# Performance work log

Hardware: AMD Instinct MI355X
Metric: run time of the kernel (lower is better)

The kernel has to match this reference:

```python
import jax, jax.numpy as jnp
import numpy as np
import math

B, T, DIM, NH, NKV, HD = 1, 2048, 1024, 16, 8, 64
N_REP = NH // NKV
LAMBDA_INIT = 0.8 - 0.6 * math.exp(-0.3)  # layer_idx = 0
EPS = 1e-5


def _rope(t, cos, sin):
    # t: (B, T, H, HD); cos/sin: (T, HD//2)
    tr = t.reshape(t.shape[:-1] + (HD // 2, 2))
    r, i = tr[..., 0], tr[..., 1]
    c = cos[None, :, None, :]
    s = sin[None, :, None, :]
    out_r = r * c - i * s
    out_i = r * s + i * c
    return jnp.stack([out_r, out_i], axis=-1).reshape(t.shape)


def setup_inputs():
    key = jax.random.key(0)
    ks = jax.random.split(key, 9)
    x = jax.random.normal(ks[0], (B, T, DIM), jnp.float32)
    inv_freq = 1.0 / (10000.0 ** (np.arange(0, HD, 2, dtype=np.float32) / HD))
    angles = np.outer(np.arange(T, dtype=np.float32), inv_freq)  # (T, HD//2)
    freqs_cos = jnp.asarray(np.cos(angles), jnp.float32)
    freqs_sin = jnp.asarray(np.sin(angles), jnp.float32)
    wq = jax.random.normal(ks[1], (2 * NH * HD, DIM), jnp.float32) * 0.02
    wk = jax.random.normal(ks[2], (2 * NKV * HD, DIM), jnp.float32) * 0.02
    wv = jax.random.normal(ks[3], (NKV * HD, DIM), jnp.float32) * 0.02
    wo = jax.random.normal(ks[4], (DIM, NH * HD), jnp.float32) * 0.02
    lambda_q1 = jax.random.normal(ks[5], (HD,), jnp.float32) * 0.1
    lambda_k1 = jax.random.normal(ks[6], (HD,), jnp.float32) * 0.1
    lambda_q2 = jax.random.normal(ks[7], (HD,), jnp.float32) * 0.1
    lambda_k2 = jax.random.normal(ks[8], (HD,), jnp.float32) * 0.1
    return dict(x=x, freqs_cos=freqs_cos, freqs_sin=freqs_sin, wq=wq, wk=wk,
                wv=wv, wo=wo, lambda_q1=lambda_q1, lambda_k1=lambda_k1,
                lambda_q2=lambda_q2, lambda_k2=lambda_k2)


def reference(x, freqs_cos, freqs_sin, wq, wk, wv, wo,
              lambda_q1, lambda_k1, lambda_q2, lambda_k2):
    Bc, Tc, C = x.shape
    q = (x @ wq.T).reshape(Bc, Tc, NH, 2, HD)
    k = (x @ wk.T).reshape(Bc, Tc, NKV, 2, HD)
    v = (x @ wv.T).reshape(Bc, Tc, NKV, HD)
    q1, q2 = q[..., 0, :], q[..., 1, :]
    k1, k2 = k[..., 0, :], k[..., 1, :]
    q1 = _rope(q1, freqs_cos, freqs_sin)
    k1 = _rope(k1, freqs_cos, freqs_sin)
    q2 = _rope(q2, freqs_cos, freqs_sin)
    k2 = _rope(k2, freqs_cos, freqs_sin)
    # GQA: repeat each kv head n_rep times consecutively
    k1 = jnp.repeat(k1, N_REP, axis=2)
    k2 = jnp.repeat(k2, N_REP, axis=2)
    v = jnp.repeat(v, N_REP, axis=2)
    # (B, H, T, HD)
    q1, q2 = jnp.swapaxes(q1, 1, 2), jnp.swapaxes(q2, 1, 2)
    k1, k2 = jnp.swapaxes(k1, 1, 2), jnp.swapaxes(k2, 1, 2)
    v = jnp.swapaxes(v, 1, 2)
    scale = 1.0 / math.sqrt(HD)
    mask = jnp.tril(jnp.ones((Tc, Tc), bool))

    def attn_probs(qh, kh):
        s = jnp.einsum('bhtd,bhsd->bhts', qh, kh) * scale
        s = jnp.where(mask[None, None], s, -jnp.inf)
        return jax.nn.softmax(s, axis=-1)

    a1 = attn_probs(q1, k1)
    a2 = attn_probs(q2, k2)
    lam = (jnp.exp(jnp.sum(lambda_q1 * lambda_k1))
           - jnp.exp(jnp.sum(lambda_q2 * lambda_k2)) + LAMBDA_INIT)
    y = jnp.einsum('bhts,bhsd->bhtd', a1 - lam * a2, v)  # (B,H,T,HD)
    y = jnp.swapaxes(y, 1, 2)  # (B,T,H,HD)
    # GroupNorm(num_groups=NH, affine=False) on (B,C,T): normalize per (batch, head)
    # over (T, HD) elements.
    mean = y.mean(axis=(1, 3), keepdims=True)
    var = y.var(axis=(1, 3), keepdims=True)
    y = (y - mean) / jnp.sqrt(var + EPS)
    y = y.reshape(Bc, Tc, C) * (1.0 - LAMBDA_INIT)
    return y @ wo.T
```

## Files before the change

### kernel.cpp

```cpp
#include <hip/hip_runtime.h>
#include <hip/hip_bf16.h>
#include <cstdint>

#define T_SEQ 2048
#define DIM   1024
#define NHEAD 16
#define NKVH  8
#define HDIM  64
#define QKVN  3584

static constexpr float LAMBDA_INIT_F = 0.3555090675909693f;
static constexpr float ONE_MINUS_LI  = 0.6444909324090307f;
static constexpr float QSCALE_EXP2   = 0.1803368801111144f;

typedef __bf16 bf16x8 __attribute__((ext_vector_type(8)));
typedef float  f32x4  __attribute__((ext_vector_type(4)));

static __device__ __forceinline__ ushort f2bf(float f) {
  union { float f; uint32_t u; } x; x.f = f;
  uint32_t u = x.u;
  uint32_t r = (u + 0x7fffu + ((u >> 16) & 1u)) >> 16;
  return (ushort)r;
}
static __device__ __forceinline__ float bf2f(ushort u) {
  union { uint32_t u; float f; } x; x.u = ((uint32_t)u) << 16; return x.f;
}
static __device__ __forceinline__ f32x4 zero4() {
  f32x4 z = {0.f, 0.f, 0.f, 0.f}; return z;
}
static __device__ __forceinline__ bf16x8 ldfrag128(const ushort* p) {
  union { bf16x8 v; uint4 u; } r;
  r.u = *(const uint4*)p;
  return r.v;
}
static __device__ __forceinline__ void gll16(const ushort* g, ushort* l) {
  __builtin_amdgcn_global_load_lds(
      (const __attribute__((address_space(1))) uint32_t*)g,
      (__attribute__((address_space(3))) uint32_t*)l, 16, 0, 0);
}

__global__ void cvt_all(const float* __restrict__ x,  const float* __restrict__ wq,
                        const float* __restrict__ wk, const float* __restrict__ wv,
                        const float* __restrict__ wo,
                        ushort* __restrict__ xb, ushort* __restrict__ Wb,
                        ushort* __restrict__ Wob) {
  int g = (blockIdx.x * 256 + threadIdx.x) * 4;
  float4 v; ushort* dst; int j;
  if (g < 2097152) {
    v = *(const float4*)(x + g); dst = xb; j = g;
  } else if (g < 5767168) {
    j = g - 2097152;
    const float* src = (j < 2097152) ? (wq + j)
                     : (j < 3145728) ? (wk + (j - 2097152))
                                     : (wv + (j - 3145728));
    v = *(const float4*)src; dst = Wb;
  } else {
    j = g - 5767168;
    v = *(const float4*)(wo + j); dst = Wob;
  }
  int q = (j & 31) >> 2;
  int jp = (j & ~31) + ((q & 3) << 3) + ((q >> 2) << 2);
  ushort4 o4;
  o4.x = f2bf(v.x); o4.y = f2bf(v.y); o4.z = f2bf(v.z); o4.w = f2bf(v.w);
  *(ushort4*)(dst + jp) = o4;
}

__global__ void lam_kernel(const float* __restrict__ lq1, const float* __restrict__ lk1,
                           const float* __restrict__ lq2, const float* __restrict__ lk2,
                           float* __restrict__ lam) {
  int lane = threadIdx.x;
  float p1 = lq1[lane] * lk1[lane];
  float p2 = lq2[lane] * lk2[lane];
  #pragma unroll
  for (int off = 32; off >= 1; off >>= 1) {
    p1 += __shfl_down(p1, off);
    p2 += __shfl_down(p2, off);
  }
  if (lane == 0) *lam = expf(p1) - expf(p2) + LAMBDA_INIT_F;
}

template<int BF16OUT>
__global__ __launch_bounds__(256) void gemm_bt(const ushort* __restrict__ A,
                                               const ushort* __restrict__ W,
                                               void* __restrict__ Cout,
                                               int M, int N, int K) {
  __shared__ __align__(16) ushort As[2 * 128 * 32];
  __shared__ __align__(16) ushort Ws[2 * 128 * 32];
  const int tid  = threadIdx.x;
  const int lane = tid & 63;
  const int w    = tid >> 6;
  const int wr   = w >> 1, wc = w & 1;
  const int nwg = gridDim.x * gridDim.y;
  int id  = blockIdx.x * gridDim.y + blockIdx.y;
  int sw  = (id & 7) * (nwg >> 3) + (id >> 3);
  const int bm = (sw % gridDim.y) * 128;
  const int bn = (sw / gridDim.y) * 128;
  const int fr = lane & 15;
  const int fg = (lane >> 4) * 4;
  const int g8 = (lane >> 4) * 8;

  f32x4 acc[4][4];
  #pragma unroll
  for (int m = 0; m < 4; ++m)
    #pragma unroll
    for (int n = 0; n < 4; ++n) acc[m][n] = zero4();

  const int col  = (lane & 3) * 8;
  const int row0 = w * 16 + (lane >> 2);
  const int row1 = row0 + 64;
  const ushort* ga0 = A + (size_t)(bm + row0) * K + col;
  const ushort* ga1 = A + (size_t)(bm + row1) * K + col;
  const ushort* gw0 = W + (size_t)(bn + row0) * K + col;
  const ushort* gw1 = W + (size_t)(bn + row1) * K + col;
  ushort* la0 = As + (w * 512);
  ushort* la1 = As + (w * 512) + 2048;
  ushort* la2 = As + 4096 + (w * 512);
  ushort* la3 = As + 4096 + (w * 512) + 2048;
  ushort* lw0 = Ws + (w * 512);
  ushort* lw1 = Ws + (w * 512) + 2048;
  ushort* lw2 = Ws + 4096 + (w * 512);
  ushort* lw3 = Ws + 4096 + (w * 512) + 2048;

  for (int k0 = 0; k0 < K; k0 += 64) {
    gll16(ga0 + k0,      la0);
    gll16(ga1 + k0,      la1);
    gll16(ga0 + k0 + 32, la2);
    gll16(ga1 + k0 + 32, la3);
    gll16(gw0 + k0,      lw0);
    gll16(gw1 + k0,      lw1);
    gll16(gw0 + k0 + 32, lw2);
    gll16(gw1 + k0 + 32, lw3);
    __syncthreads();
    #pragma unroll
    for (int kk = 0; kk < 2; ++kk) {
      bf16x8 af[4], bfr[4];
      #pragma unroll
      for (int m = 0; m < 4; ++m)
        af[m]  = ldfrag128(&As[kk*4096 + (wr*64 + m*16 + fr) * 32 + g8]);
      #pragma unroll
      for (int n = 0; n < 4; ++n)
        bfr[n] = ldfrag128(&Ws[kk*4096 + (wc*64 + n*16 + fr) * 32 + g8]);
      #pragma unroll
      for (int m = 0; m < 4; ++m)
        #pragma unroll
        for (int n = 0; n < 4; ++n)
          acc[m][n] = __builtin_amdgcn_mfma_f32_16x16x32_bf16(af[m], bfr[n], acc[m][n], 0, 0, 0);
    }
    __syncthreads();
  }

  #pragma unroll
  for (int m = 0; m < 4; ++m)
    #pragma unroll
    for (int n = 0; n < 4; ++n)
      #pragma unroll
      for (int i = 0; i < 4; ++i) {
        int row = bm + wr*64 + m*16 + fg + i;
        int colg = bn + wc*64 + n*16 + fr;
        float v = acc[m][n][i];
        if (BF16OUT) ((ushort*)Cout)[(size_t)row * N + colg] = f2bf(v);
        else         ((float*)Cout)[(size_t)row * N + colg]  = v;
      }
}

__global__ void reorg(const ushort* __restrict__ QKV, ushort* __restrict__ Qr,
                      ushort* __restrict__ Kr, ushort* __restrict__ Vt,
                      const float* __restrict__ fc, const float* __restrict__ fs) {
  int idx = blockIdx.x * 256 + threadIdx.x;
  if (idx < 786432) {
    int nheads, col_off; ushort* dst; float scale; int id;
    if (idx < 524288) { id = idx * 4; nheads = NHEAD; col_off = 0; dst = Qr; scale = QSCALE_EXP2; }
    else { id = (idx - 524288) * 4; nheads = NKVH; col_off = 2048; dst = Kr; scale = 1.0f; }
    int per_t = nheads * 64;
    int t  = id / per_t;
    int r  = id - t * per_t;
    int hh = r >> 6;
    int c2 = (r >> 5) & 1;
    int j  = r & 31;
    int cl = col_off + hh * 128 + c2 * 64 + 2 * j;
    uint4 raw = *(const uint4*)(QKV + (size_t)t * QKVN + cl);
    const ushort* rp = (const ushort*)&raw;
    float c4[4], s4[4];
    *(float4*)c4 = *(const float4*)(fc + t * 32 + j);
    *(float4*)s4 = *(const float4*)(fs + t * 32 + j);
    ushort outv[8];
    #pragma unroll
    for (int p = 0; p < 4; ++p) {
      float rv = bf2f(rp[2*p]), iv = bf2f(rp[2*p + 1]);
      outv[2*p]     = f2bf((rv * c4[p] - iv * s4[p]) * scale);
      outv[2*p + 1] = f2bf((rv * s4[p] + iv * c4[p]) * scale);
    }
    int d0 = 2 * j;
    int o  = d0 & 31;
    int q0 = o >> 2;
    int s0 = ((q0 & 3) << 3) + ((q0 >> 2) << 2);
    int s1 = (((q0+1) & 3) << 3) + (((q0+1) >> 2) << 2);
    size_t ob = ((size_t)(c2 * nheads + hh) * T_SEQ + t) * HDIM + (d0 & ~31);
    *(uint2*)(dst + ob + s0) = *(const uint2*)(outv);
    *(uint2*)(dst + ob + s1) = *(const uint2*)(outv + 4);
  } else {
    int id = (idx - 786432) * 8;
    int t = id & (T_SEQ - 1);
    int rest = id >> 11;
    ushort outv[8];
    #pragma unroll
    for (int p = 0; p < 8; ++p) outv[p] = QKV[(size_t)(t + p) * QKVN + 3072 + rest];
    int o  = t & 31;
    int q0 = o >> 2;
    int s0 = ((q0 & 3) << 3) + ((q0 >> 2) << 2);
    int s1 = (((q0+1) & 3) << 3) + (((q0+1) >> 2) << 2);
    size_t ob = (size_t)rest * T_SEQ + (t & ~31);
    *(uint2*)(Vt + ob + s0) = *(const uint2*)(outv);
    *(uint2*)(Vt + ob + s1) = *(const uint2*)(outv + 4);
  }
}

__global__ __launch_bounds__(256, 2) void attn_kernel(const ushort* __restrict__ Qr,
                                                      const ushort* __restrict__ Kr,
                                                      const ushort* __restrict__ Vt,
                                                      const float* __restrict__ lamp,
                                                      float* __restrict__ Yf,
                                                      float* __restrict__ part) {
  const int bx = blockIdx.x;
  const int h  = bx & 15;
  const int jb = bx >> 4;
  const int qb = (jb < 16) ? (31 - jb) : (jb - 16);
  const int kh = h >> 1;
  const int tid = threadIdx.x;
  const int lane = tid & 63;
  const int w   = tid >> 6;
  const int st  = w >> 1;
  const int qh  = w & 1;
  const int fr  = lane & 15;
  const int fg  = (lane >> 4) * 4;
  const int g8  = (lane >> 4) * 8;

  __shared__ float ob[64 * 64];
  __shared__ float sb[8];

  bf16x8 qf[2][2];
  #pragma unroll
  for (int qs = 0; qs < 2; ++qs) {
    const int row = qb * 64 + qh * 32 + qs * 16 + fr;
    const ushort* qp = Qr + ((size_t)(st * NHEAD + h) * T_SEQ + row) * HDIM;
    qf[qs][0] = ldfrag128(qp + g8);
    qf[qs][1] = ldfrag128(qp + 32 + g8);
  }

  float m_[2] = {-__builtin_inff(), -__builtin_inff()};
  float l_[2] = {0.f, 0.f};
  f32x4 o_[2][4];
  #pragma unroll
  for (int qs = 0; qs < 2; ++qs)
    #pragma unroll
    for (int dn = 0; dn < 4; ++dn) o_[qs][dn] = zero4();

  const ushort* Kbase = Kr + ((size_t)(st * NKVH + kh) * T_SEQ + fr) * HDIM + g8;
  const ushort* Vbase = Vt + ((size_t)(kh * 64 + fr) * T_SEQ) + g8;

#define SINGLE_TILE(KT, DOMASK) do {                                          \
    const int kvb_ = (KT) * 64;                                               \
    bf16x8 kf_[4][2], vf_[4][2];                                              \
    _Pragma("unroll")                                                         \
    for (int n_ = 0; n_ < 4; ++n_) {                                          \
      const ushort* kp_ = Kbase + (size_t)(kvb_ + n_ * 16) * HDIM;            \
      kf_[n_][0] = ldfrag128(kp_);                                            \
      kf_[n_][1] = ldfrag128(kp_ + 32);                                       \
      const ushort* vp_ = Vbase + (size_t)(n_ * 16) * T_SEQ + kvb_;           \
      vf_[n_][0] = ldfrag128(vp_);                                            \
      vf_[n_][1] = ldfrag128(vp_ + 32);                                       \
    }                                                                         \
    float sv_[2][4][4];                                                       \
    __builtin_amdgcn_s_setprio(1);                                            \
    _Pragma("unroll")                                                         \
    for (int n_ = 0; n_ < 4; ++n_) {                                          \
      f32x4 a0_ = zero4(), a1_ = zero4();                                     \
      _Pragma("unroll")                                                       \
      for (int ks_ = 0; ks_ < 2; ++ks_) {                                     \
        a0_ = __builtin_amdgcn_mfma_f32_16x16x32_bf16(kf_[n_][ks_], qf[0][ks_], a0_, 0, 0, 0); \
        a1_ = __builtin_amdgcn_mfma_f32_16x16x32_bf16(kf_[n_][ks_], qf[1][ks_], a1_, 0, 0, 0); \
      }                                                                       \
      _Pragma("unroll")                                                       \
      for (int i_ = 0; i_ < 4; ++i_) { sv_[0][n_][i_] = a0_[i_]; sv_[1][n_][i_] = a1_[i_]; } \
    }                                                                         \
    __builtin_amdgcn_s_setprio(0);                                            \
    if (DOMASK) {                                                             \
      _Pragma("unroll")                                                       \
      for (int qs_ = 0; qs_ < 2; ++qs_) {                                     \
        const int qloc_ = qh*32 + qs_*16 + fr;                                \
        _Pragma("unroll")                                                     \
        for (int n_ = 0; n_ < 4; ++n_)                                        \
          _Pragma("unroll")                                                   \
          for (int i_ = 0; i_ < 4; ++i_)                                      \
            if (n_*16 + fg + i_ > qloc_) sv_[qs_][n_][i_] = -__builtin_inff();\
      }                                                                       \
    }                                                                         \
    bf16x8 pa_[2][2];                                                         \
    _Pragma("unroll")                                                         \
    for (int qs_ = 0; qs_ < 2; ++qs_) {                                       \
      float rm_ = -__builtin_inff();                                          \
      _Pragma("unroll")                                                       \
      for (int n_ = 0; n_ < 4; ++n_)                                          \
        _Pragma("unroll")                                                     \
        for (int i_ = 0; i_ < 4; ++i_) rm_ = fmaxf(rm_, sv_[qs_][n_][i_]);    \
      rm_ = fmaxf(rm_, __shfl_xor(rm_, 16));                                  \
      rm_ = fmaxf(rm_, __shfl_xor(rm_, 32));                                  \
      if (!__all(rm_ <= m_[qs_] + 8.f)) {                                     \
        float mnew_ = fmaxf(m_[qs_], rm_);                                    \
        float sc_ = __builtin_amdgcn_exp2f(m_[qs_] - mnew_);                  \
        m_[qs_] = mnew_;                                                      \
        l_[qs_] *= sc_;                                                       \
        float scs_[4];                                                        \
        _Pragma("unroll")                                                     \
        for (int i_ = 0; i_ < 4; ++i_) scs_[i_] = __shfl(sc_, fg + i_);       \
        _Pragma("unroll")                                                     \
        for (int dn_ = 0; dn_ < 4; ++dn_)                                     \
          _Pragma("unroll")                                                   \
          for (int i_ = 0; i_ < 4; ++i_) o_[qs_][dn_][i_] *= scs_[i_];        \
      }                                                                       \
      float rs_ = 0.f;                                                        \
      _Pragma("unroll")                                                       \
      for (int n_ = 0; n_ < 4; ++n_)                                          \
        _Pragma("unroll")                                                     \
        for (int i_ = 0; i_ < 4; ++i_) {                                      \
          float p_ = __builtin_amdgcn_exp2f(sv_[qs_][n_][i_] - m_[qs_]);      \
          sv_[qs_][n_][i_] = p_; rs_ += p_;                                   \
        }                                                                     \
      rs_ += __shfl_xor(rs_, 16);                                             \
      rs_ += __shfl_xor(rs_, 32);                                             \
      l_[qs_] += rs_;                                                         \
      _Pragma("unroll")                                                       \
      for (int ks_ = 0; ks_ < 2; ++ks_)                                       \
        _Pragma("unroll")                                                     \
        for (int n2_ = 0; n2_ < 2; ++n2_)                                     \
          _Pragma("unroll")                                                   \
          for (int i_ = 0; i_ < 4; ++i_)                                      \
            pa_[qs_][ks_][n2_*4 + i_] = (__bf16)sv_[qs_][2*ks_ + n2_][i_];    \
    }                                                                         \
    __builtin_amdgcn_s_setprio(1);                                            \
    _Pragma("unroll")                                                         \
    for (int ks_ = 0; ks_ < 2; ++ks_)                                         \
      _Pragma("unroll")                                                       \
      for (int dn_ = 0; dn_ < 4; ++dn_) {                                     \
        o_[0][dn_] = __builtin_amdgcn_mfma_f32_16x16x32_bf16(pa_[0][ks_], vf_[dn_][ks_], o_[0][dn_], 0, 0, 0); \
        o_[1][dn_] = __builtin_amdgcn_mfma_f32_16x16x32_bf16(pa_[1][ks_], vf_[dn_][ks_], o_[1][dn_], 0, 0, 0); \
      }                                                                       \
    __builtin_amdgcn_s_setprio(0);                                            \
  } while (0)

  const int nnd = qb;
  int kt = 0;
  for (; kt + 1 < nnd; kt += 2) {
    const int ka = kt * 64, kb = ka + 64;
    bf16x8 kfA[4][2], vfA[4][2], kfB[4][2], vfB[4][2];
    #pragma unroll
    for (int n = 0; n < 4; ++n) {
      const ushort* kpA = Kbase + (size_t)(ka + n * 16) * HDIM;
      const ushort* kpB = Kbase + (size_t)(kb + n * 16) * HDIM;
      kfA[n][0] = ldfrag128(kpA);  kfA[n][1] = ldfrag128(kpA + 32);
      kfB[n][0] = ldfrag128(kpB);  kfB[n][1] = ldfrag128(kpB + 32);
      const ushort* vpA = Vbase + (size_t)(n * 16) * T_SEQ + ka;
      vfA[n][0] = ldfrag128(vpA);  vfA[n][1] = ldfrag128(vpA + 32);
      const ushort* vpB = vpA + 64;
      vfB[n][0] = ldfrag128(vpB);  vfB[n][1] = ldfrag128(vpB + 32);
    }
    float svA[2][4][4], svB[2][4][4];
    __builtin_amdgcn_s_setprio(1);
    #pragma unroll
    for (int n = 0; n < 4; ++n) {
      f32x4 a0 = zero4(), a1 = zero4(), b0 = zero4(), b1 = zero4();
      #pragma unroll
      for (int ks = 0; ks < 2; ++ks) {
        a0 = __builtin_amdgcn_mfma_f32_16x16x32_bf16(kfA[n][ks], qf[0][ks], a0, 0, 0, 0);
        a1 = __builtin_amdgcn_mfma_f32_16x16x32_bf16(kfA[n][ks], qf[1][ks], a1, 0, 0, 0);
        b0 = __builtin_amdgcn_mfma_f32_16x16x32_bf16(kfB[n][ks], qf[0][ks], b0, 0, 0, 0);
        b1 = __builtin_amdgcn_mfma_f32_16x16x32_bf16(kfB[n][ks], qf[1][ks], b1, 0, 0, 0);
      }
      #pragma unroll
      for (int i = 0; i < 4; ++i) {
        svA[0][n][i] = a0[i]; svA[1][n][i] = a1[i];
        svB[0][n][i] = b0[i]; svB[1][n][i] = b1[i];
      }
    }
    __builtin_amdgcn_s_setprio(0);

    bf16x8 paA[2][2], paB[2][2];
    #pragma unroll
    for (int qs = 0; qs < 2; ++qs) {
      float rm = -__builtin_inff();
      #pragma unroll
      for (int n = 0; n < 4; ++n)
        #pragma unroll
        for (int i = 0; i < 4; ++i) {
          rm = fmaxf(rm, svA[qs][n][i]);
          rm = fmaxf(rm, svB[qs][n][i]);
        }
      rm = fmaxf(rm, __shfl_xor(rm, 16));
      rm = fmaxf(rm, __shfl_xor(rm, 32));
      if (!__all(rm <= m_[qs] + 8.f)) {
        float mnew = fmaxf(m_[qs], rm);
        float sc = __builtin_amdgcn_exp2f(m_[qs] - mnew);
        m_[qs] = mnew;
        l_[qs] *= sc;
        float scs[4];
        #pragma unroll
        for (int i = 0; i < 4; ++i) scs[i] = __shfl(sc, fg + i);
        #pragma unroll
        for (int dn = 0; dn < 4; ++dn)
          #pragma unroll
          for (int i = 0; i < 4; ++i) o_[qs][dn][i] *= scs[i];
      }
      float rs = 0.f;
      #pragma unroll
      for (int n = 0; n < 4; ++n)
        #pragma unroll
        for (int i = 0; i < 4; ++i) {
          float pA = __builtin_amdgcn_exp2f(svA[qs][n][i] - m_[qs]);
          float pB = __builtin_amdgcn_exp2f(svB[qs][n][i] - m_[qs]);
          svA[qs][n][i] = pA; svB[qs][n][i] = pB;
          rs += pA + pB;
        }
      rs += __shfl_xor(rs, 16);
      rs += __shfl_xor(rs, 32);
      l_[qs] += rs;
      #pragma unroll
      for (int ks = 0; ks < 2; ++ks)
        #pragma unroll
        for (int n2 = 0; n2 < 2; ++n2)
          #pragma unroll
          for (int i = 0; i < 4; ++i) {
            paA[qs][ks][n2*4 + i] = (__bf16)svA[qs][2*ks + n2][i];
            paB[qs][ks][n2*4 + i] = (__bf16)svB[qs][2*ks + n2][i];
          }
    }

    __builtin_amdgcn_s_setprio(1);
    #pragma unroll
    for (int ks = 0; ks < 2; ++ks)
      #pragma unroll
      for (int dn = 0; dn < 4; ++dn) {
        o_[0][dn] = __builtin_amdgcn_mfma_f32_16x16x32_bf16(paA[0][ks], vfA[dn][ks], o_[0][dn], 0, 0, 0);
        o_[1][dn] = __builtin_amdgcn_mfma_f32_16x16x32_bf16(paA[1][ks], vfA[dn][ks], o_[1][dn], 0, 0, 0);
      }
    #pragma unroll
    for (int ks = 0; ks < 2; ++ks)
      #pragma unroll
      for (int dn = 0; dn < 4; ++dn) {
        o_[0][dn] = __builtin_amdgcn_mfma_f32_16x16x32_bf16(paB[0][ks], vfB[dn][ks], o_[0][dn], 0, 0, 0);
        o_[1][dn] = __builtin_amdgcn_mfma_f32_16x16x32_bf16(paB[1][ks], vfB[dn][ks], o_[1][dn], 0, 0, 0);
      }
    __builtin_amdgcn_s_setprio(0);
  }
  if (kt < nnd) { SINGLE_TILE(kt, 0); ++kt; }
  SINGLE_TILE(qb, 1);
#undef SINGLE_TILE

  float iq[2][4];
  #pragma unroll
  for (int qs = 0; qs < 2; ++qs) {
    float inv = __builtin_amdgcn_rcpf(l_[qs]);
    #pragma unroll
    for (int i = 0; i < 4; ++i) iq[qs][i] = __shfl(inv, fg + i);
  }
  __syncthreads();
  if (st == 1) {
    #pragma unroll
    for (int qs = 0; qs < 2; ++qs)
      #pragma unroll
      for (int dn = 0; dn < 4; ++dn)
        #pragma unroll
        for (int i = 0; i < 4; ++i)
          ob[(qh*32 + qs*16 + fg + i)*64 + dn*16 + fr] = o_[qs][dn][i] * iq[qs][i];
  }
  __syncthreads();
  if (st == 0) {
    const float lam = *lamp;
    float s = 0.f, s2 = 0.f;
    #pragma unroll
    for (int qs = 0; qs < 2; ++qs)
      #pragma unroll
      for (int dn = 0; dn < 4; ++dn)
        #pragma unroll
        for (int i = 0; i < 4; ++i) {
          int r64 = qh*32 + qs*16 + fg + i;
          int d   = dn*16 + fr;
          float v = o_[qs][dn][i] * iq[qs][i] - lam * ob[r64*64 + d];
          Yf[(size_t)(qb*64 + r64) * DIM + h*64 + d] = v;
          s += v; s2 += v * v;
        }
    #pragma unroll
    for (int off = 1; off <= 32; off <<= 1) {
      s  += __shfl_xor(s, off);
      s2 += __shfl_xor(s2, off);
    }
    if (lane == 0) { sb[w] = s; sb[4 + w] = s2; }
  }
  __syncthreads();
  if (tid == 0) {
    part[bx]       = sb[0] + sb[1];
    part[512 + bx] = sb[4] + sb[5];
  }
}

__global__ void stats_final(const float* __restrict__ part, float* __restrict__ stat) {
  int hh = threadIdx.x;
  if (hh < 16) {
    float S = 0.f, S2 = 0.f;
    #pragma unroll
    for (int j = 0; j < 32; ++j) { S += part[j*16 + hh]; S2 += part[512 + j*16 + hh]; }
    const float N = (float)(T_SEQ * HDIM);
    float mean = S / N;
    float var  = S2 / N - mean * mean;
    stat[hh]      = mean;
    stat[16 + hh] = rsqrtf(var + 1e-5f);
  }
}

__global__ void norm_cvt(const float* __restrict__ Y, const float* __restrict__ stats,
                         ushort* __restrict__ Yb) {
  int idx = (blockIdx.x * 256 + threadIdx.x) * 4;
  int col = idx & (DIM - 1);
  int h = col >> 6;
  float mean = stats[h], isd = stats[16 + h] * ONE_MINUS_LI;
  float4 v = *(const float4*)(Y + idx);
  ushort4 o4;
  o4.x = f2bf((v.x - mean) * isd);
  o4.y = f2bf((v.y - mean) * isd);
  o4.z = f2bf((v.z - mean) * isd);
  o4.w = f2bf((v.w - mean) * isd);
  int q = (col & 31) >> 2;
  int idxp = (idx & ~31) + ((q & 3) << 3) + ((q >> 2) << 2);
  *(ushort4*)(Yb + idxp) = o4;
}

extern "C" void kernel_launch(void* const* d_in, const int* in_sizes, int n_in,
                              void* d_out, int out_size, void* d_ws, size_t ws_size,
                              hipStream_t stream) {
  const float* x   = (const float*)d_in[0];
  const float* fc  = (const float*)d_in[1];
  const float* fs  = (const float*)d_in[2];
  const float* wq  = (const float*)d_in[3];
  const float* wk  = (const float*)d_in[4];
  const float* wv  = (const float*)d_in[5];
  const float* wo  = (const float*)d_in[6];
  const float* lq1 = (const float*)d_in[7];
  const float* lk1 = (const float*)d_in[8];
  const float* lq2 = (const float*)d_in[9];
  const float* lk2 = (const float*)d_in[10];
  float* out = (float*)d_out;

  char* ws = (char*)d_ws;
  const size_t OFF_WOB  = 0;
  const size_t OFF_XB   = 2097152;
  const size_t OFF_WB   = 6291456;
  const size_t OFF_QKV  = 13631488;
  const size_t OFF_QR   = 28311552;
  const size_t OFF_KR   = 36700160;
  const size_t OFF_VT   = 40894464;
  const size_t OFF_Y    = 18874368;
  const size_t OFF_YB   = 42991616;
  const size_t OFF_ST   = 47185920;

  ushort* xb   = (ushort*)(ws + OFF_XB);
  ushort* Wb   = (ushort*)(ws + OFF_WB);
  ushort* Wob  = (ushort*)(ws + OFF_WOB);
  ushort* QKVb = (ushort*)(ws + OFF_QKV);
  ushort* Qr   = (ushort*)(ws + OFF_QR);
  ushort* Kr   = (ushort*)(ws + OFF_KR);
  ushort* Vt   = (ushort*)(ws + OFF_VT);
  float*  Yf   = (float*)(ws + OFF_Y);
  ushort* Yb   = (ushort*)(ws + OFF_YB);
  float*  stat = (float*)(ws + OFF_ST);
  float*  lamp = stat + 32;
  float*  part = stat + 64;

  cvt_all<<<6656, 256, 0, stream>>>(x, wq, wk, wv, wo, xb, Wb, Wob);
  lam_kernel<<<1, 64, 0, stream>>>(lq1, lk1, lq2, lk2, lamp);

  gemm_bt<1><<<dim3(QKVN/128, T_SEQ/128), 256, 0, stream>>>(xb, Wb, QKVb, T_SEQ, QKVN, DIM);

  reorg<<<3584, 256, 0, stream>>>(QKVb, Qr, Kr, Vt, fc, fs);

  attn_kernel<<<512, 256, 0, stream>>>(Qr, Kr, Vt, lamp, Yf, part);

  stats_final<<<1, 64, 0, stream>>>(part, stat);
  norm_cvt<<<2048, 256, 0, stream>>>(Yf, stat, Yb);

  gemm_bt<0><<<dim3(DIM/128, T_SEQ/128), 256, 0, stream>>>(Yb, Wob, out, T_SEQ, DIM, DIM);
}
```

Measured before the change: 141.2 us.

## Store Q/K/V in MFMA fragment-tiled layout for contiguous per-lane loads

The RoPE/transpose prep kernel now writes Q, K and V into a layout where each 16-row MFMA fragment occupies a contiguous 512-element block, ordered so that lane*8 addresses a full 16-byte fragment. The attention kernel then loads Q, K and V fragments as fully coalesced contiguous 1KB wave reads rather than strided row reads. This reduces scattered global memory transactions in the attention inner loop. The cost is a more complex index mapping in the prep kernel, with scattered 8-byte writes there.

```diff
diff --git a/kernel.cpp b/kernel.cpp
--- a/kernel.cpp
+++ b/kernel.cpp
@@ -190,28 +190,30 @@
       outv[2*p]     = f2bf((rv * c4[p] - iv * s4[p]) * scale);
       outv[2*p + 1] = f2bf((rv * s4[p] + iv * c4[p]) * scale);
     }
-    int d0 = 2 * j;
-    int o  = d0 & 31;
-    int q0 = o >> 2;
-    int s0 = ((q0 & 3) << 3) + ((q0 >> 2) << 2);
-    int s1 = (((q0+1) & 3) << 3) + (((q0+1) >> 2) << 2);
-    size_t ob = ((size_t)(c2 * nheads + hh) * T_SEQ + t) * HDIM + (d0 & ~31);
-    *(uint2*)(dst + ob + s0) = *(const uint2*)(outv);
-    *(uint2*)(dst + ob + s1) = *(const uint2*)(outv + 4);
+    int d0  = 2 * j;
+    int ks  = (d0 >> 5) & 1;
+    int dlo = d0 & 31;
+    int gb  = (dlo >> 2) & 2;
+    int e   = (dlo & 16) >> 2;
+    size_t base = ((size_t)(c2 * nheads + hh) * T_SEQ + (t & ~15)) * HDIM
+                + ks * 512 + (t & 15) * 8;
+    *(uint2*)(dst + base + gb * 128 + e)        = *(const uint2*)(outv);
+    *(uint2*)(dst + base + (gb + 1) * 128 + e)  = *(const uint2*)(outv + 4);
   } else {
     int id = (idx - 786432) * 8;
     int t = id & (T_SEQ - 1);
     int rest = id >> 11;
+    int kh = rest >> 6, d = rest & 63;
     ushort outv[8];
     #pragma unroll
     for (int p = 0; p < 8; ++p) outv[p] = QKV[(size_t)(t + p) * QKVN + 3072 + rest];
-    int o  = t & 31;
-    int q0 = o >> 2;
-    int s0 = ((q0 & 3) << 3) + ((q0 >> 2) << 2);
-    int s1 = (((q0+1) & 3) << 3) + (((q0+1) >> 2) << 2);
-    size_t ob = (size_t)rest * T_SEQ + (t & ~31);
-    *(uint2*)(Vt + ob + s0) = *(const uint2*)(outv);
-    *(uint2*)(Vt + ob + s1) = *(const uint2*)(outv + 4);
+    int tlo = t & 31;
+    int gb  = (tlo >> 2) & 2;
+    int e   = (tlo & 16) >> 2;
+    size_t base = (size_t)kh * (64 * T_SEQ)
+                + ((size_t)((t >> 5) * 4 + (d >> 4))) * 512 + (d & 15) * 8;
+    *(uint2*)(Vt + base + gb * 128 + e)        = *(const uint2*)(outv);
+    *(uint2*)(Vt + base + (gb + 1) * 128 + e)  = *(const uint2*)(outv + 4);
   }
 }
 
@@ -233,7 +235,6 @@
   const int qh  = w & 1;
   const int fr  = lane & 15;
   const int fg  = (lane >> 4) * 4;
-  const int g8  = (lane >> 4) * 8;
 
   __shared__ float ob[64 * 64];
   __shared__ float sb[8];
@@ -241,10 +242,10 @@
   bf16x8 qf[2][2];
   #pragma unroll
   for (int qs = 0; qs < 2; ++qs) {
-    const int row = qb * 64 + qh * 32 + qs * 16 + fr;
-    const ushort* qp = Qr + ((size_t)(st * NHEAD + h) * T_SEQ + row) * HDIM;
-    qf[qs][0] = ldfrag128(qp + g8);
-    qf[qs][1] = ldfrag128(qp + 32 + g8);
+    const ushort* qp = Qr + (size_t)(st * NHEAD + h) * (T_SEQ * HDIM)
+                     + (size_t)(qb * 4 + qh * 2 + qs) * 1024 + lane * 8;
+    qf[qs][0] = ldfrag128(qp);
+    qf[qs][1] = ldfrag128(qp + 512);
   }
 
   float m_[2] = {-__builtin_inff(), -__builtin_inff()};
@@ -255,20 +256,23 @@
     #pragma unroll
     for (int dn = 0; dn < 4; ++dn) o_[qs][dn] = zero4();
 
-  const ushort* Kbase = Kr + ((size_t)(st * NKVH + kh) * T_SEQ + fr) * HDIM + g8;
-  const ushort* Vbase = Vt + ((size_t)(kh * 64 + fr) * T_SEQ) + g8;
+  const ushort* Kbase = Kr + (size_t)(st * NKVH + kh) * (T_SEQ * HDIM) + lane * 8;
+  const ushort* Vbase = Vt + (size_t)kh * (64 * T_SEQ) + lane * 8;
 
 #define SINGLE_TILE(KT, DOMASK) do {                                          \
-    const int kvb_ = (KT) * 64;                                               \
     bf16x8 kf_[4][2], vf_[4][2];                                              \
     _Pragma("unroll")                                                         \
     for (int n_ = 0; n_ < 4; ++n_) {                                          \
-      const ushort* kp_ = Kbase + (size_t)(kvb_ + n_ * 16) * HDIM;            \
+      const ushort* kp_ = Kbase + (size_t)((KT) * 4 + n_) * 1024;             \
       kf_[n_][0] = ldfrag128(kp_);                                            \
-      kf_[n_][1] = ldfrag128(kp_ + 32);                                       \
-      const ushort* vp_ = Vbase + (size_t)(n_ * 16) * T_SEQ + kvb_;           \
-      vf_[n_][0] = ldfrag128(vp_);                                            \
-      vf_[n_][1] = ldfrag128(vp_ + 32);                                       \
+      kf_[n_][1] = ldfrag128(kp_ + 512);                                      \
+    }                                                                         \
+    _Pragma("unroll")                                                         \
+    for (int ks_ = 0; ks_ < 2; ++ks_) {                                       \
+      const ushort* vp_ = Vbase + (size_t)(((KT) * 2 + ks_) * 4) * 512;       \
+      _Pragma("unroll")                                                       \
+      for (int dn_ = 0; dn_ < 4; ++dn_)                                       \
+        vf_[dn_][ks_] = ldfrag128(vp_ + dn_ * 512);                           \
     }                                                                         \
     float sv_[2][4][4];                                                       \
     __builtin_amdgcn_s_setprio(1);                                            \
@@ -351,18 +355,23 @@
   const int nnd = qb;
   int kt = 0;
   for (; kt + 1 < nnd; kt += 2) {
-    const int ka = kt * 64, kb = ka + 64;
     bf16x8 kfA[4][2], vfA[4][2], kfB[4][2], vfB[4][2];
     #pragma unroll
     for (int n = 0; n < 4; ++n) {
-      const ushort* kpA = Kbase + (size_t)(ka + n * 16) * HDIM;
-      const ushort* kpB = Kbase + (size_t)(kb + n * 16) * HDIM;
-      kfA[n][0] = ldfrag128(kpA);  kfA[n][1] = ldfrag128(kpA + 32);
-      kfB[n][0] = ldfrag128(kpB);  kfB[n][1] = ldfrag128(kpB + 32);
-      const ushort* vpA = Vbase + (size_t)(n * 16) * T_SEQ + ka;
-      vfA[n][0] = ldfrag128(vpA);  vfA[n][1] = ldfrag128(vpA + 32);
-      const ushort* vpB = vpA + 64;
-      vfB[n][0] = ldfrag128(vpB);  vfB[n][1] = ldfrag128(vpB + 32);
+      const ushort* kpA = Kbase + (size_t)(kt * 4 + n) * 1024;
+      const ushort* kpB = kpA + 4096;
+      kfA[n][0] = ldfrag128(kpA);  kfA[n][1] = ldfrag128(kpA + 512);
+      kfB[n][0] = ldfrag128(kpB);  kfB[n][1] = ldfrag128(kpB + 512);
+    }
+    #pragma unroll
+    for (int ks = 0; ks < 2; ++ks) {
+      const ushort* vpA = Vbase + (size_t)((kt * 2 + ks) * 4) * 512;
+      const ushort* vpB = vpA + 4096;
+      #pragma unroll
+      for (int dn = 0; dn < 4; ++dn) {
+        vfA[dn][ks] = ldfrag128(vpA + dn * 512);
+        vfB[dn][ks] = ldfrag128(vpB + dn * 512);
+      }
     }
     float svA[2][4][4], svB[2][4][4];
     __builtin_amdgcn_s_setprio(1);
```

Result: faster. 117.4 us (-16.9%).
